# Performance work log

Measured on AMD Instinct MI355X. Metric: run time of the kernel, lower is better.

The kernel has to match this reference:

```python
import jax, jax.numpy as jnp
import numpy as np

A_CONST = 0.1
B_CONST = 0.2
C_CONST = 0.8

INPUT_SIZE = 1024
HIDDEN_SIZE = 2048
BATCH = 32768
SIGMA = 0.02


def acti_func(x, a, b, c):
    # piecewise: a*(1 - x/b) for x<=b ; 0 for b<x<c ; a*(x-c)/(1-c) for x>=c
    low = -a * x / b + a
    high = a * x / (1.0 - c) + a * c / (c - 1.0)
    return jnp.where(x <= b, low, jnp.where(x >= c, high, jnp.zeros_like(x)))


def setup_inputs() -> dict:
    key = jax.random.key(0)
    ks = jax.random.split(key, 4)
    x = jax.random.normal(ks[0], (BATCH, INPUT_SIZE), dtype=jnp.float32)
    W0 = jax.random.normal(ks[1], (INPUT_SIZE, HIDDEN_SIZE), dtype=jnp.float32) * SIGMA
    b0 = jnp.zeros((HIDDEN_SIZE,), dtype=jnp.float32)
    W1 = jax.random.normal(ks[2], (HIDDEN_SIZE, HIDDEN_SIZE), dtype=jnp.float32) * SIGMA
    b1 = jnp.zeros((HIDDEN_SIZE,), dtype=jnp.float32)
    W2 = jax.random.normal(ks[3], (HIDDEN_SIZE, 1), dtype=jnp.float32) * SIGMA
    b2 = jnp.zeros((1,), dtype=jnp.float32)
    return {"x": x, "W0": W0, "b0": b0, "W1": W1, "b1": b1, "W2": W2, "b2": b2}


def reference(x, W0, b0, W1, b1, W2, b2):
    h = jax.nn.elu(x @ W0 + b0)
    h = jax.nn.elu(h @ W1 + b1)
    out = jax.nn.sigmoid(h @ W2 + b2)  # [B, 1]
    alpha = acti_func(out, A_CONST, B_CONST, C_CONST)
    return out, alpha
```

## Files before the change

### kernel.cpp

```cpp
#include <hip/hip_runtime.h>
#include <hip/hip_bf16.h>
#include <stdint.h>

typedef unsigned short u16;
typedef __bf16 bf16x8 __attribute__((ext_vector_type(8)));
typedef float floatx4 __attribute__((ext_vector_type(4)));

__device__ __forceinline__ u16 f2bf(float f) {
  union { float f; unsigned u; } c; c.f = f;
  unsigned r = c.u + 0x7fffu + ((c.u >> 16) & 1u);
  return (u16)(r >> 16);
}

__device__ __forceinline__ void load_lds16(const void* g, void* l) {
  __builtin_amdgcn_global_load_lds(
      (const __attribute__((address_space(1))) void*)g,
      (__attribute__((address_space(3))) void*)l,
      16, 0, 0);
}

__device__ __forceinline__ void memclob() { asm volatile("" ::: "memory"); }
__device__ __forceinline__ void barrier_() {
  memclob();
  __builtin_amdgcn_s_barrier();
  memclob();
}

__global__ __launch_bounds__(256) void preamble(
    const float* __restrict__ x, const float* __restrict__ W0,
    const float* __restrict__ W1,
    u16* __restrict__ Xb, u16* __restrict__ Wt0, u16* __restrict__ Wt1,
    float* __restrict__ z)
{
  __shared__ float tile[32][33];
  const int bid = blockIdx.x;
  const int t = threadIdx.x;

  if (bid < 32768) {
    int i = bid * 256 + t;
    float4 f = ((const float4*)x)[i];
    ushort4 u;
    u.x = f2bf(f.x); u.y = f2bf(f.y); u.z = f2bf(f.z); u.w = f2bf(f.w);
    ((ushort4*)Xb)[i] = u;
  } else if (bid < 32768 + 2048) {
    int tb = bid - 32768;
    int bx = (tb & 63) * 32, by = (tb >> 6) * 32;
    int tx = t & 31, ty = t >> 5;
    #pragma unroll
    for (int i = 0; i < 32; i += 8)
      tile[ty + i][tx] = W0[(size_t)(by + ty + i) * 2048 + bx + tx];
    __syncthreads();
    #pragma unroll
    for (int i = 0; i < 32; i += 8)
      Wt0[(size_t)(bx + ty + i) * 1024 + by + tx] = f2bf(tile[tx][ty + i]);
  } else if (bid < 32768 + 2048 + 4096) {
    int tb = bid - (32768 + 2048);
    int bx = (tb & 63) * 32, by = (tb >> 6) * 32;
    int tx = t & 31, ty = t >> 5;
    #pragma unroll
    for (int i = 0; i < 32; i += 8)
      tile[ty + i][tx] = W1[(size_t)(by + ty + i) * 2048 + bx + tx];
    __syncthreads();
    #pragma unroll
    for (int i = 0; i < 32; i += 8)
      Wt1[(size_t)(bx + ty + i) * 2048 + by + tx] = f2bf(tile[tx][ty + i]);
  } else {
    int tb = bid - (32768 + 2048 + 4096);
    ((float4*)z)[tb * 256 + t] = (float4){0.f, 0.f, 0.f, 0.f};
  }
}

template<bool FUSE_HEAD, int KK>
__global__ __launch_bounds__(512, 2) void gemm256_r2(
    const u16* __restrict__ A,
    const u16* __restrict__ Bt,
    const float* __restrict__ bias,
    u16* __restrict__ C,
    const float* __restrict__ W2,
    float* __restrict__ z,
    int M, int N)
{
  __shared__ u16 lds[65536];

  const int t = threadIdx.x;
  const int l = t & 63;
  const int w = t >> 6;
  const int wm = w >> 2;
  const int wn = w & 3;
  const int lm = l & 15;
  const int q  = l >> 4;

  const int nwg = gridDim.x;
  int wg = blockIdx.x;
  wg = (wg & 7) * (nwg >> 3) + (wg >> 3);
  const int nbn = N >> 8;
  const int n0 = (wg % nbn) << 8;
  const int m0 = (wg / nbn) << 8;

  const int rowoff = t >> 3;
  const int lc8 = ((t & 7) ^ (rowoff & 7)) * 8;
  const int bq = rowoff >> 5;
  const int br = rowoff & 31;
  const u16* rA0 = A  + (size_t)(m0 + rowoff) * KK + lc8;
  const u16* rA1 = A  + (size_t)(m0 + 128 + rowoff) * KK + lc8;
  const u16* rB0 = Bt + (size_t)(n0 + bq * 64 + br) * KK + lc8;
  const u16* rB1 = Bt + (size_t)(n0 + (2 + bq) * 64 + br) * KK + lc8;
  const int ldst = t * 8;

#define SLOT(p, idx) (((p) * 4 + (idx)) * 8192)

#define STG_A(P, S, KOFF) do {                                                 \
    load_lds16(rA0 + (S) * 64 * KK + (KOFF), &lds[SLOT(P, S) + ldst]);         \
    load_lds16(rA1 + (S) * 64 * KK + (KOFF), &lds[SLOT(P, S) + 4096 + ldst]);  \
  } while (0)
#define STG_B(P, S, KOFF) do {                                                 \
    load_lds16(rB0 + (S) * 32 * KK + (KOFF), &lds[SLOT(P, 2 + (S)) + ldst]);   \
    load_lds16(rB1 + (S) * 32 * KK + (KOFF), &lds[SLOT(P, 2 + (S)) + 4096 + ldst]); \
  } while (0)

  const int ck0 = ((0 * 4 + q) ^ (lm & 7)) * 8;
  const int ck1 = ((1 * 4 + q) ^ (lm & 7)) * 8;
  const int arow = (wm * 64 + lm) * 64;
  const int brow = (wn * 32 + lm) * 64;
#define RDA(p, i, ck) (*(const bf16x8*)&lds[SLOT(p, (i) >> 2) + arow + ((i) & 3) * 1024 + (ck)])
#define RDB(p, j, ck) (*(const bf16x8*)&lds[SLOT(p, 2 + ((j) >> 1)) + brow + ((j) & 1) * 1024 + (ck)])
#define MFMA(d, x, y) d = __builtin_amdgcn_mfma_f32_16x16x32_bf16(x, y, d, 0, 0, 0)

  floatx4 acc[8][4];
  #pragma unroll
  for (int i = 0; i < 8; ++i)
    #pragma unroll
    for (int j = 0; j < 4; ++j)
      acc[i][j] = (floatx4){0.f, 0.f, 0.f, 0.f};

  bf16x8 a0[4][2];
  bf16x8 a1[4][2];
  bf16x8 bl[2][2];
  bf16x8 bh[2][2];

  constexpr int NK = KK >> 6;
  static_assert(NK >= 4 && (NK & 1) == 0, "NK must be even, >= 4");

#define VMW6 asm volatile("s_waitcnt vmcnt(6)" ::: "memory")
#define VMW0 asm volatile("s_waitcnt vmcnt(0)" ::: "memory")
#define VMWN do {} while (0)

#define KTILE2(P, SAH, KO1, S2, KO2, VMW)                                      \
  {                                                                            \
    barrier_();                   \
    _Pragma("unroll")                                                          \
    for (int i = 0; i < 4; ++i) { a0[i][0] = RDA(P, i, ck0); a0[i][1] = RDA(P, i, ck1); } \
    _Pragma("unroll")                                                          \
    for (int j = 0; j < 2; ++j) { bl[j][0] = RDB(P, j, ck0); bl[j][1] = RDB(P, j, ck1); } \
    _Pragma("unroll")                                                          \
    for (int j = 0; j < 2; ++j) { bh[j][0] = RDB(P, 2 + j, ck0); bh[j][1] = RDB(P, 2 + j, ck1); } \
    if (SAH) { STG_A((P) ^ 1, 1, KO1); }                                       \
    __builtin_amdgcn_s_setprio(1);                                             \
    _Pragma("unroll")                                                          \
    for (int i = 0; i < 4; ++i)                                                \
      _Pragma("unroll")                                                        \
      for (int j = 0; j < 2; ++j) {                                            \
        MFMA(acc[i][j], a0[i][0], bl[j][0]);                                   \
        MFMA(acc[i][j], a0[i][1], bl[j][1]);                                   \
      }                                                                        \
    _Pragma("unroll")                                                          \
    for (int i = 0; i < 4; ++i)                                                \
      _Pragma("unroll")                                                        \
      for (int j = 0; j < 2; ++j) {                                            \
        MFMA(acc[i][2 + j], a0[i][0], bh[j][0]);                               \
        MFMA(acc[i][2 + j], a0[i][1], bh[j][1]);                               \
      }                                                                        \
    __builtin_amdgcn_s_setprio(0);                                             \
    barrier_();                   \
    _Pragma("unroll")                                                          \
    for (int i = 0; i < 4; ++i) { a1[i][0] = RDA(P, 4 + i, ck0); a1[i][1] = RDA(P, 4 + i, ck1); } \
    if (S2) { STG_A(P, 0, KO2); STG_B(P, 0, KO2); STG_B(P, 1, KO2); }          \
    __builtin_amdgcn_s_setprio(1);                                             \
    _Pragma("unroll")                                                          \
    for (int i = 0; i < 4; ++i)                                                \
      _Pragma("unroll")                                                        \
      for (int j = 0; j < 2; ++j) {                                            \
        MFMA(acc[4 + i][j], a1[i][0], bl[j][0]);                               \
        MFMA(acc[4 + i][j], a1[i][1], bl[j][1]);                               \
      }                                                                        \
    _Pragma("unroll")                                                          \
    for (int i = 0; i < 4; ++i)                                                \
      _Pragma("unroll")                                                        \
      for (int j = 0; j < 2; ++j) {                                            \
        MFMA(acc[4 + i][2 + j], a1[i][0], bh[j][0]);                           \
        MFMA(acc[4 + i][2 + j], a1[i][1], bh[j][1]);                           \
      }                                                                        \
    __builtin_amdgcn_s_setprio(0);                                             \
    VMW;                                                                       \
  }

  STG_A(0, 0, 0); memclob(); STG_A(0, 1, 0); memclob();
  STG_B(0, 0, 0); memclob(); STG_B(0, 1, 0); memclob();
  STG_A(1, 0, 64); memclob(); STG_B(1, 0, 64); memclob(); STG_B(1, 1, 64);
  VMW6;

  #pragma unroll 1
  for (int g = 0; g < NK - 2; g += 2) {
    KTILE2(0, true, 64, true, 128, VMW6);
    KTILE2(1, true, 128, true, 192, VMW6);
    rA0 += 128; rA1 += 128; rB0 += 128; rB1 += 128;
  }
  KTILE2(0, true, 64, false, 0, VMW0);
  KTILE2(1, false, 0, false, 0, VMWN);

  float bv[4];
  #pragma unroll
  for (int j = 0; j < 4; ++j) bv[j] = bias[n0 + wn * 64 + j * 16 + lm];

  if (!FUSE_HEAD) {
    #pragma unroll
    for (int i = 0; i < 8; ++i) {
      #pragma unroll
      for (int r = 0; r < 4; ++r) {
        int grow = m0 + wm * 128 + i * 16 + q * 4 + r;
        size_t base = (size_t)grow * N + n0 + wn * 64 + lm;
        #pragma unroll
        for (int j = 0; j < 4; ++j) {
          float v = acc[i][j][r] + bv[j];
          v = v > 0.f ? v : (__expf(v) - 1.f);
          C[base + j * 16] = f2bf(v);
        }
      }
    }
  } else {
    float w2v[4];
    #pragma unroll
    for (int j = 0; j < 4; ++j) w2v[j] = W2[n0 + wn * 64 + j * 16 + lm];
    #pragma unroll
    for (int i = 0; i < 8; ++i) {
      #pragma unroll
      for (int r = 0; r < 4; ++r) {
        float pacc = 0.f;
        #pragma unroll
        for (int j = 0; j < 4; ++j) {
          float v = acc[i][j][r] + bv[j];
          v = v > 0.f ? v : (__expf(v) - 1.f);
          pacc += v * w2v[j];
        }
        pacc += __shfl_xor(pacc, 1);
        pacc += __shfl_xor(pacc, 2);
        pacc += __shfl_xor(pacc, 4);
        pacc += __shfl_xor(pacc, 8);
        if (lm == 0) atomicAdd(&z[m0 + wm * 128 + i * 16 + q * 4 + r], pacc);
      }
    }
  }
#undef SLOT
#undef STG_A
#undef STG_B
#undef RDA
#undef RDB
#undef MFMA
#undef KTILE2
#undef VMW6
#undef VMW0
#undef VMWN
}

__global__ __launch_bounds__(256) void sigmoid_alpha(
    const float* __restrict__ z, const float* __restrict__ b2,
    float* __restrict__ out, int B)
{
  int i = blockIdx.x * blockDim.x + threadIdx.x;
  if (i >= B) return;
  float o = 1.f / (1.f + expf(-(z[i] + b2[0])));
  float alpha;
  if (o <= 0.2f)      alpha = 0.1f - 0.5f * o;
  else if (o >= 0.8f) alpha = 0.5f * o - 0.4f;
  else                alpha = 0.f;
  out[i] = o;
  out[B + i] = alpha;
}

extern "C" void kernel_launch(void* const* d_in, const int* in_sizes, int n_in,
                              void* d_out, int out_size, void* d_ws, size_t ws_size,
                              hipStream_t stream) {
  const int BATCH = 32768, HID = 2048;

  const float* x  = (const float*)d_in[0];
  const float* W0 = (const float*)d_in[1];
  const float* b0 = (const float*)d_in[2];
  const float* W1 = (const float*)d_in[3];
  const float* b1 = (const float*)d_in[4];
  const float* W2 = (const float*)d_in[5];
  const float* b2 = (const float*)d_in[6];
  float* out = (float*)d_out;

  char* ws = (char*)d_ws;
  u16* Xb   = (u16*)(ws);
  u16* Wt0  = (u16*)(ws + (size_t)67108864);
  u16* Wt1  = (u16*)(ws + (size_t)71303168);
  u16* h0   = (u16*)(ws + (size_t)79691776);
  float* z  = (float*)(ws + (size_t)213909504);

  const int grid = (BATCH / 256) * (HID / 256);

  preamble<<<32768 + 2048 + 4096 + 32, 256, 0, stream>>>(x, W0, W1, Xb, Wt0, Wt1, z);
  gemm256_r2<false, 1024><<<grid, 512, 0, stream>>>(
      Xb, Wt0, b0, h0, nullptr, nullptr, BATCH, HID);
  gemm256_r2<true, 2048><<<grid, 512, 0, stream>>>(
      h0, Wt1, b1, nullptr, W2, z, BATCH, HID);
  sigmoid_alpha<<<BATCH / 256, 256, 0, stream>>>(z, b2, out, BATCH);
}
```

Before: 588.1 us.

## Shrink GEMM tile to 128x256 with BK=32 double buffering for higher occupancy

Replaces the 256x256 tile with BK=64 and a split two-phase pipeline by a 128x256 tile with BK=32, a simple LDS double buffer and a full vmcnt(0) wait each k-step. LDS use drops sharply, and launch bounds now ask for 4 workgroups per CU, so more waves can hide latency. The cost is lower arithmetic intensity per tile, more barriers per unit of K, and loss of the finer-grained prefetch overlap, which may hurt MFMA utilisation.

```diff
diff --git a/kernel.cpp b/kernel.cpp
--- a/kernel.cpp
+++ b/kernel.cpp
@@ -71,7 +71,7 @@
 }
 
 template<bool FUSE_HEAD, int KK>
-__global__ __launch_bounds__(512, 2) void gemm256_r2(
+__global__ __launch_bounds__(512, 4) void gemm128x256(
     const u16* __restrict__ A,
     const u16* __restrict__ Bt,
     const float* __restrict__ bias,
@@ -80,7 +80,7 @@
     float* __restrict__ z,
     int M, int N)
 {
-  __shared__ u16 lds[65536];
+  __shared__ u16 lds[2][12288];
 
   const int t = threadIdx.x;
   const int l = t & 63;
@@ -95,118 +95,69 @@
   wg = (wg & 7) * (nwg >> 3) + (wg >> 3);
   const int nbn = N >> 8;
   const int n0 = (wg % nbn) << 8;
-  const int m0 = (wg / nbn) << 8;
-
-  const int rowoff = t >> 3;
-  const int lc8 = ((t & 7) ^ (rowoff & 7)) * 8;
-  const int bq = rowoff >> 5;
-  const int br = rowoff & 31;
-  const u16* rA0 = A  + (size_t)(m0 + rowoff) * KK + lc8;
-  const u16* rA1 = A  + (size_t)(m0 + 128 + rowoff) * KK + lc8;
-  const u16* rB0 = Bt + (size_t)(n0 + bq * 64 + br) * KK + lc8;
-  const u16* rB1 = Bt + (size_t)(n0 + (2 + bq) * 64 + br) * KK + lc8;
+  const int m0 = (wg / nbn) << 7;
+
+  const int srow = t >> 2;
+  const int lc8 = ((t & 3) ^ ((t >> 3) & 3)) * 8;
+  const u16* rA = A  + (size_t)(m0 + srow) * KK + lc8;
+  const u16* rB = Bt + (size_t)(n0 + srow) * KK + lc8;
   const int ldst = t * 8;
 
-#define SLOT(p, idx) (((p) * 4 + (idx)) * 8192)
-
-#define STG_A(P, S, KOFF) do {                                                 \
-    load_lds16(rA0 + (S) * 64 * KK + (KOFF), &lds[SLOT(P, S) + ldst]);         \
-    load_lds16(rA1 + (S) * 64 * KK + (KOFF), &lds[SLOT(P, S) + 4096 + ldst]);  \
+#define STG(P, KOFF) do {                                                      \
+    load_lds16(rA + (KOFF), &lds[P][ldst]);                                    \
+    load_lds16(rB + (KOFF), &lds[P][4096 + ldst]);                             \
+    load_lds16(rB + 128 * KK + (KOFF), &lds[P][8192 + ldst]);                  \
   } while (0)
-#define STG_B(P, S, KOFF) do {                                                 \
-    load_lds16(rB0 + (S) * 32 * KK + (KOFF), &lds[SLOT(P, 2 + (S)) + ldst]);   \
-    load_lds16(rB1 + (S) * 32 * KK + (KOFF), &lds[SLOT(P, 2 + (S)) + 4096 + ldst]); \
-  } while (0)
-
-  const int ck0 = ((0 * 4 + q) ^ (lm & 7)) * 8;
-  const int ck1 = ((1 * 4 + q) ^ (lm & 7)) * 8;
-  const int arow = (wm * 64 + lm) * 64;
-  const int brow = (wn * 32 + lm) * 64;
-#define RDA(p, i, ck) (*(const bf16x8*)&lds[SLOT(p, (i) >> 2) + arow + ((i) & 3) * 1024 + (ck)])
-#define RDB(p, j, ck) (*(const bf16x8*)&lds[SLOT(p, 2 + ((j) >> 1)) + brow + ((j) & 1) * 1024 + (ck)])
+
+  const int ck = (q ^ ((lm >> 1) & 3)) * 8;
+  const int arow = (wm * 64 + lm) * 32;
+  const int brow = 4096 + (wn * 64 + lm) * 32;
+#define RDA(p, i) (*(const bf16x8*)&lds[p][arow + (i) * 512 + ck])
+#define RDB(p, j) (*(const bf16x8*)&lds[p][brow + (j) * 512 + ck])
 #define MFMA(d, x, y) d = __builtin_amdgcn_mfma_f32_16x16x32_bf16(x, y, d, 0, 0, 0)
 
-  floatx4 acc[8][4];
+  floatx4 acc[4][4];
   #pragma unroll
-  for (int i = 0; i < 8; ++i)
+  for (int i = 0; i < 4; ++i)
     #pragma unroll
     for (int j = 0; j < 4; ++j)
       acc[i][j] = (floatx4){0.f, 0.f, 0.f, 0.f};
 
-  bf16x8 a0[4][2];
-  bf16x8 a1[4][2];
-  bf16x8 bl[2][2];
-  bf16x8 bh[2][2];
-
-  constexpr int NK = KK >> 6;
+  constexpr int NK = KK >> 5;
   static_assert(NK >= 4 && (NK & 1) == 0, "NK must be even, >= 4");
 
-#define VMW6 asm volatile("s_waitcnt vmcnt(6)" ::: "memory")
 #define VMW0 asm volatile("s_waitcnt vmcnt(0)" ::: "memory")
-#define VMWN do {} while (0)
-
-#define KTILE2(P, SAH, KO1, S2, KO2, VMW)                                      \
+
+#define TILE(P, DOSTG, KOFF, DOVMW)                                            \
   {                                                                            \
-    barrier_();                   \
+    barrier_();                                                                \
+    if (DOSTG) { STG((P) ^ 1, KOFF); }                                         \
+    bf16x8 a_[4], b_[4];                                                       \
     _Pragma("unroll")                                                          \
-    for (int i = 0; i < 4; ++i) { a0[i][0] = RDA(P, i, ck0); a0[i][1] = RDA(P, i, ck1); } \
+    for (int i = 0; i < 4; ++i) a_[i] = RDA(P, i);                             \
     _Pragma("unroll")                                                          \
-    for (int j = 0; j < 2; ++j) { bl[j][0] = RDB(P, j, ck0); bl[j][1] = RDB(P, j, ck1); } \
-    _Pragma("unroll")                                                          \
-    for (int j = 0; j < 2; ++j) { bh[j][0] = RDB(P, 2 + j, ck0); bh[j][1] = RDB(P, 2 + j, ck1); } \
-    if (SAH) { STG_A((P) ^ 1, 1, KO1); }                                       \
+    for (int j = 0; j < 4; ++j) b_[j] = RDB(P, j);                             \
     __builtin_amdgcn_s_setprio(1);                                             \
     _Pragma("unroll")                                                          \
     for (int i = 0; i < 4; ++i)                                                \
       _Pragma("unroll")                                                        \
-      for (int j = 0; j < 2; ++j) {                                            \
-        MFMA(acc[i][j], a0[i][0], bl[j][0]);                                   \
-        MFMA(acc[i][j], a0[i][1], bl[j][1]);                                   \
-      }                                                                        \
-    _Pragma("unroll")                                                          \
-    for (int i = 0; i < 4; ++i)                                                \
-      _Pragma("unroll")                                                        \
-      for (int j = 0; j < 2; ++j) {                                            \
-        MFMA(acc[i][2 + j], a0[i][0], bh[j][0]);                               \
-        MFMA(acc[i][2 + j], a0[i][1], bh[j][1]);                               \
-      }                                                                        \
+      for (int j = 0; j < 4; ++j)                                              \
+        MFMA(acc[i][j], a_[i], b_[j]);                                         \
     __builtin_amdgcn_s_setprio(0);                                             \
-    barrier_();                   \
-    _Pragma("unroll")                                                          \
-    for (int i = 0; i < 4; ++i) { a1[i][0] = RDA(P, 4 + i, ck0); a1[i][1] = RDA(P, 4 + i, ck1); } \
-    if (S2) { STG_A(P, 0, KO2); STG_B(P, 0, KO2); STG_B(P, 1, KO2); }          \
-    __builtin_amdgcn_s_setprio(1);                                             \
-    _Pragma("unroll")                                                          \
-    for (int i = 0; i < 4; ++i)                                                \
-      _Pragma("unroll")                                                        \
-      for (int j = 0; j < 2; ++j) {                                            \
-        MFMA(acc[4 + i][j], a1[i][0], bl[j][0]);                               \
-        MFMA(acc[4 + i][j], a1[i][1], bl[j][1]);                               \
-      }                                                                        \
-    _Pragma("unroll")                                                          \
-    for (int i = 0; i < 4; ++i)                                                \
-      _Pragma("unroll")                                                        \
-      for (int j = 0; j < 2; ++j) {                                            \
-        MFMA(acc[4 + i][2 + j], a1[i][0], bh[j][0]);                           \
-        MFMA(acc[4 + i][2 + j], a1[i][1], bh[j][1]);                           \
-      }                                                                        \
-    __builtin_amdgcn_s_setprio(0);                                             \
-    VMW;                                                                       \
-  }
-
-  STG_A(0, 0, 0); memclob(); STG_A(0, 1, 0); memclob();
-  STG_B(0, 0, 0); memclob(); STG_B(0, 1, 0); memclob();
-  STG_A(1, 0, 64); memclob(); STG_B(1, 0, 64); memclob(); STG_B(1, 1, 64);
-  VMW6;
+    if (DOVMW) { VMW0; }                                                       \
+  }
+
+  STG(0, 0);
+  VMW0;
 
   #pragma unroll 1
   for (int g = 0; g < NK - 2; g += 2) {
-    KTILE2(0, true, 64, true, 128, VMW6);
-    KTILE2(1, true, 128, true, 192, VMW6);
-    rA0 += 128; rA1 += 128; rB0 += 128; rB1 += 128;
-  }
-  KTILE2(0, true, 64, false, 0, VMW0);
-  KTILE2(1, false, 0, false, 0, VMWN);
+    TILE(0, true, 32, true);
+    TILE(1, true, 64, true);
+    rA += 64; rB += 64;
+  }
+  TILE(0, true, 32, true);
+  TILE(1, false, 0, false);
 
   float bv[4];
   #pragma unroll
@@ -214,10 +165,10 @@
 
   if (!FUSE_HEAD) {
     #pragma unroll
-    for (int i = 0; i < 8; ++i) {
+    for (int i = 0; i < 4; ++i) {
       #pragma unroll
       for (int r = 0; r < 4; ++r) {
-        int grow = m0 + wm * 128 + i * 16 + q * 4 + r;
+        int grow = m0 + wm * 64 + i * 16 + q * 4 + r;
         size_t base = (size_t)grow * N + n0 + wn * 64 + lm;
         #pragma unroll
         for (int j = 0; j < 4; ++j) {
@@ -232,7 +183,7 @@
     #pragma unroll
     for (int j = 0; j < 4; ++j) w2v[j] = W2[n0 + wn * 64 + j * 16 + lm];
     #pragma unroll
-    for (int i = 0; i < 8; ++i) {
+    for (int i = 0; i < 4; ++i) {
       #pragma unroll
       for (int r = 0; r < 4; ++r) {
         float pacc = 0.f;
@@ -246,20 +197,16 @@
         pacc += __shfl_xor(pacc, 2);
         pacc += __shfl_xor(pacc, 4);
         pacc += __shfl_xor(pacc, 8);
-        if (lm == 0) atomicAdd(&z[m0 + wm * 128 + i * 16 + q * 4 + r], pacc);
+        if (lm == 0) atomicAdd(&z[m0 + wm * 64 + i * 16 + q * 4 + r], pacc);
       }
     }
   }
-#undef SLOT
-#undef STG_A
-#undef STG_B
+#undef STG
 #undef RDA
 #undef RDB
 #undef MFMA
-#undef KTILE2
-#undef VMW6
+#undef TILE
 #undef VMW0
-#undef VMWN
 }
 
 __global__ __launch_bounds__(256) void sigmoid_alpha(
@@ -298,12 +245,12 @@
   u16* h0   = (u16*)(ws + (size_t)79691776);
   float* z  = (float*)(ws + (size_t)213909504);
 
-  const int grid = (BATCH / 256) * (HID / 256);
+  const int grid = (HID / 256) * (BATCH / 128);
 
   preamble<<<32768 + 2048 + 4096 + 32, 256, 0, stream>>>(x, W0, W1, Xb, Wt0, Wt1, z);
-  gemm256_r2<false, 1024><<<grid, 512, 0, stream>>>(
+  gemm128x256<false, 1024><<<grid, 512, 0, stream>>>(
       Xb, Wt0, b0, h0, nullptr, nullptr, BATCH, HID);
-  gemm256_r2<true, 2048><<<grid, 512, 0, stream>>>(
+  gemm128x256<true, 2048><<<grid, 512, 0, stream>>>(
       h0, Wt1, b1, nullptr, W2, z, BATCH, HID);
   sigmoid_alpha<<<BATCH / 256, 256, 0, stream>>>(z, b2, out, BATCH);
 }
```

Result: slower. 647.3 us (+10.1%).
